# Kernel optimization log

Measured on AMD Instinct MI355X. Metric: run time of the kernel, lower is better.

Reference implementation:

```python
import jax, jax.numpy as jnp
import numpy as np

SEQ_LEN = 4096
DIM = 256  # hidden_dim, must be even


def rope_tables(seq_len, dim):
    half = dim // 2
    pos = jnp.arange(seq_len, dtype=jnp.float32)[:, None]  # (s,1)
    div = jnp.exp(jnp.arange(half, dtype=jnp.float32) * (-jnp.log(jnp.float32(10000.0)) / half))
    ang = pos * div  # (s, half)
    return jnp.sin(ang), jnp.cos(ang)


def apply_rope(x, sin, cos):
    # x: (b, s, d); sin/cos: (s, d//2). Interleaved pair rotation.
    b, s, d = x.shape
    xp = x.reshape(b, s, d // 2, 2)
    x_even, x_odd = xp[..., 0], xp[..., 1]
    out_even = x_even * cos - x_odd * sin
    out_odd = x_even * sin + x_odd * cos
    return jnp.stack([out_even, out_odd], axis=-1).reshape(b, s, d)


def setup_inputs() -> dict:
    key = jax.random.key(0)
    k1, k2, k3, k4 = jax.random.split(key, 4)
    x = jax.random.normal(k1, (4, SEQ_LEN, DIM), dtype=jnp.float32)
    W0 = jax.random.normal(k2, (DIM, DIM), dtype=jnp.float32)
    W1 = jax.random.normal(k3, (DIM, DIM), dtype=jnp.float32)
    W2 = jax.random.normal(k4, (DIM, DIM), dtype=jnp.float32)
    return {"x": x, "W0": W0, "W1": W1, "W2": W2}


def reference(x, W0, W1, W2):
    sin, cos = rope_tables(x.shape[1], W0.shape[1])
    x0 = apply_rope(jnp.einsum('bsi,ih->bsh', x, W0), sin, cos)  # (b,s,h)
    x1 = apply_rope(jnp.einsum('bsi,ih->bsh', x, W1), sin, cos)  # (b,s,h)
    scores = jnp.einsum('bsh,bth->bst', x0, x1)                   # (b,s,s)
    attn = jax.nn.softmax(scores, axis=-1)
    x2 = jnp.einsum('bsh,ho->bso', x, W2)                         # (b,s,o)
    out = jnp.einsum('bst,bto->bso', attn, x2)
    return out[:, 0, :]
```

## Files before the change

kernel.cpp:

```cpp
#include <hip/hip_runtime.h>
#include <math.h>

#define BB 4
#define SS 4096
#define DD 256
#define WT_PLANE 65536

typedef __attribute__((ext_vector_type(8))) _Float16 h8v;
typedef __attribute__((ext_vector_type(4))) float f4v;

__device__ __forceinline__ ushort f2h(float f) {
    _Float16 h = (_Float16)f;
    return __builtin_bit_cast(ushort, h);
}
__device__ __forceinline__ float h2f(ushort u) {
    return (float)__builtin_bit_cast(_Float16, u);
}
__device__ __forceinline__ void split2htwo(float a, float b, uint& h, uint& l) {
    const ushort ah = f2h(a);
    const ushort al = f2h(a - h2f(ah));
    const ushort bh = f2h(b);
    const ushort bl = f2h(b - h2f(bh));
    h = (uint)ah | ((uint)bh << 16);
    l = (uint)al | ((uint)bl << 16);
}

__global__ __launch_bounds__(256) void prep_kernel(const float* __restrict__ x,
                                                   const float* __restrict__ W0,
                                                   const float* __restrict__ W1,
                                                   float* __restrict__ q,
                                                   float* __restrict__ y,
                                                   float* __restrict__ out,
                                                   ushort* __restrict__ wt,
                                                   float* __restrict__ cs) {
    __shared__ float sh[64 * 65];
    const int bid = blockIdx.x;
    const int tid = threadIdx.x;

    if (bid < 2048) {
        const int t = ((bid & 63) << 6) | (tid & 63);
        const int j = ((bid >> 6) << 2) | (tid >> 6);
        const float kfac = (float)(-9.210340371976184 / 128.0);
        const float d = expf((float)j * kfac);
        float sv, cv;
        sincosf((float)t * d, &sv, &cv);
        *(float2*)(cs + ((size_t)j * SS + t) * 2) = make_float2(cv, sv);
    } else if (bid < 2080) {
        const int qb = bid - 2048;
        const int b = qb >> 3;
        const int hc = qb & 7;
        if (hc == 0) y[b * DD + tid] = 0.f;
        if (hc == 1) out[b * DD + tid] = 0.f;
        const int hk = tid & 31;
        const int iseg = tid >> 5;
        const int h = hc * 32 + hk;
        const float* xrow = x + (size_t)b * SS * DD;
        float p = 0.f;
#pragma unroll
        for (int k = 0; k < 32; ++k) {
            const int i = iseg * 32 + k;
            p = fmaf(xrow[i], W0[i * DD + h], p);
        }
        sh[tid] = p;
        __syncthreads();
        if (tid < 32) {
            float s = 0.f;
#pragma unroll
            for (int jj = 0; jj < 8; ++jj) s += sh[jj * 32 + tid];
            q[b * DD + hc * 32 + tid] = s;
        }
    } else {
        const int cb = bid - 2080;
        const int k0 = (cb & 3) * 64;
        const int c0 = (cb >> 2) * 64;
        {
            const int kr = tid >> 2;
            const int csg = tid & 3;
            const float* src = W1 + (size_t)(k0 + kr) * DD + c0 + csg * 16;
#pragma unroll
            for (int i = 0; i < 4; ++i) {
                const float4 v = *(const float4*)(src + i * 4);
                sh[kr * 65 + csg * 16 + i * 4 + 0] = v.x;
                sh[kr * 65 + csg * 16 + i * 4 + 1] = v.y;
                sh[kr * 65 + csg * 16 + i * 4 + 2] = v.z;
                sh[kr * 65 + csg * 16 + i * 4 + 3] = v.w;
            }
        }
        __syncthreads();
        {
            const int cr = tid >> 2;
            const int ks2 = tid & 3;
            const int c = c0 + cr;
#pragma unroll
            for (int oct = 0; oct < 2; ++oct) {
                const int k = k0 + ks2 * 16 + oct * 8;
                const int kl = ks2 * 16 + oct * 8;
                uint H[4], L[4];
#pragma unroll
                for (int i = 0; i < 4; ++i) {
                    const float fa = sh[(kl + 2 * i + 0) * 65 + cr];
                    const float fb = sh[(kl + 2 * i + 1) * 65 + cr];
                    split2htwo(fa, fb, H[i], L[i]);
                }
                const size_t idx = ((size_t)(c >> 4) * 8 + (k >> 5)) * 512
                                 + (size_t)((k >> 3) & 3) * 128 + (size_t)(c & 15) * 8;
                *(uint4*)(wt + idx) = make_uint4(H[0], H[1], H[2], H[3]);
                *(uint4*)(wt + WT_PLANE + idx) = make_uint4(L[0], L[1], L[2], L[3]);
            }
        }
    }
}

__global__ __launch_bounds__(1024, 4) void scores_mfma(const float* __restrict__ x,
                                                       const ushort* __restrict__ wt,
                                                       const float* __restrict__ q,
                                                       const float* __restrict__ cs,
                                                       float* __restrict__ scores) {
    __shared__ __align__(16) unsigned char smem[65536];
    __shared__ float scomb[8][64];
    __shared__ float q_s[256];
    const int tid = threadIdx.x;
    const int bid = blockIdx.x;
    const int b = bid >> 6;
    const int row0 = (bid & 63) << 6;

    if (tid < 256) q_s[tid] = q[b * DD + tid];

    {
        const int r = tid >> 4;
        const int seg = tid & 15;
        const float* xr = x + ((size_t)(b * SS + row0 + r)) * DD + seg * 16;
        const int swz = (r & 15) << 4;
#pragma unroll
        for (int j = 0; j < 2; ++j) {
            const float4 f0 = *(const float4*)(xr + j * 8);
            const float4 f1 = *(const float4*)(xr + j * 8 + 4);
            uint H[4], L[4];
            split2htwo(f0.x, f0.y, H[0], L[0]);
            split2htwo(f0.z, f0.w, H[1], L[1]);
            split2htwo(f1.x, f1.y, H[2], L[2]);
            split2htwo(f1.z, f1.w, H[3], L[3]);
            const int s = seg * 2 + j;
            const int off = r * 512 + (((s << 4)) ^ swz);
            *(uint4*)(smem + off) = make_uint4(H[0], H[1], H[2], H[3]);
            *(uint4*)(smem + 32768 + off) = make_uint4(L[0], L[1], L[2], L[3]);
        }
    }
    __syncthreads();

    const int lane = tid & 63;
    const int wv = tid >> 6;
    const int rh = wv >> 3;
    const int cg = wv & 7;
    const int l15 = lane & 15;
    const int hg = lane >> 4;

    f4v acc[2][2];
#pragma unroll
    for (int rt = 0; rt < 2; ++rt)
#pragma unroll
        for (int ct = 0; ct < 2; ++ct) acc[rt][ct] = {0.f, 0.f, 0.f, 0.f};

    const ushort* wb = wt + (size_t)lane * 8;
    const int aswz = l15 << 4;

#pragma unroll
    for (int ks = 0; ks < 8; ++ks) {
        h8v a_h[2], a_l[2];
#pragma unroll
        for (int rt = 0; rt < 2; ++rt) {
            const int row = rh * 32 + rt * 16 + l15;
            const int off = row * 512 + ((((ks * 4 + hg) << 4)) ^ aswz);
            a_h[rt] = *(const h8v*)(smem + off);
            a_l[rt] = *(const h8v*)(smem + 32768 + off);
        }
#pragma unroll
        for (int ct = 0; ct < 2; ++ct) {
            const int gct = cg * 2 + ct;
            const ushort* bp = wb + (size_t)(gct * 8 + ks) * 512;
            const h8v b_h = *(const h8v*)(bp);
            const h8v b_l = *(const h8v*)(bp + WT_PLANE);
#pragma unroll
            for (int rt = 0; rt < 2; ++rt) {
                acc[rt][ct] = __builtin_amdgcn_mfma_f32_16x16x32_f16(a_h[rt], b_h, acc[rt][ct], 0, 0, 0);
                acc[rt][ct] = __builtin_amdgcn_mfma_f32_16x16x32_f16(a_h[rt], b_l, acc[rt][ct], 0, 0, 0);
                acc[rt][ct] = __builtin_amdgcn_mfma_f32_16x16x32_f16(a_l[rt], b_h, acc[rt][ct], 0, 0, 0);
            }
        }
    }

    const int par = l15 & 1;
    float p[2][4];
#pragma unroll
    for (int rt = 0; rt < 2; ++rt)
#pragma unroll
        for (int i = 0; i < 4; ++i) p[rt][i] = 0.f;

#pragma unroll
    for (int ct = 0; ct < 2; ++ct) {
        const int c = (cg * 2 + ct) * 16 + l15;
        const int j = c >> 1;
        const float qe = q_s[2 * j], qo = q_s[2 * j + 1];
        const float* csp = cs + (size_t)j * (SS * 2);
#pragma unroll
        for (int rt = 0; rt < 2; ++rt) {
            const int t0 = row0 + rh * 32 + rt * 16 + hg * 4;
            const float4 csA = *(const float4*)(csp + t0 * 2);
            const float4 csB = *(const float4*)(csp + t0 * 2 + 4);
            const float u0 = par ? (qo * csA.x - qe * csA.y) : (qe * csA.x + qo * csA.y);
            const float u1 = par ? (qo * csA.z - qe * csA.w) : (qe * csA.z + qo * csA.w);
            const float u2 = par ? (qo * csB.x - qe * csB.y) : (qe * csB.x + qo * csB.y);
            const float u3 = par ? (qo * csB.z - qe * csB.w) : (qe * csB.z + qo * csB.w);
            p[rt][0] = fmaf(acc[rt][ct][0], u0, p[rt][0]);
            p[rt][1] = fmaf(acc[rt][ct][1], u1, p[rt][1]);
            p[rt][2] = fmaf(acc[rt][ct][2], u2, p[rt][2]);
            p[rt][3] = fmaf(acc[rt][ct][3], u3, p[rt][3]);
        }
    }
#pragma unroll
    for (int rt = 0; rt < 2; ++rt) {
#pragma unroll
        for (int off = 1; off <= 8; off <<= 1) {
            p[rt][0] += __shfl_xor(p[rt][0], off);
            p[rt][1] += __shfl_xor(p[rt][1], off);
            p[rt][2] += __shfl_xor(p[rt][2], off);
            p[rt][3] += __shfl_xor(p[rt][3], off);
        }
        if (l15 == 0)
            *(float4*)&scomb[cg][rh * 32 + rt * 16 + hg * 4] =
                make_float4(p[rt][0], p[rt][1], p[rt][2], p[rt][3]);
    }
    __syncthreads();
    if (tid < 64) {
        float s = 0.f;
#pragma unroll
        for (int g = 0; g < 8; ++g) s += scomb[g][tid];
        scores[(size_t)b * SS + row0 + tid] = s;
    }
}

__global__ __launch_bounds__(256) void fused_kernel(const float* __restrict__ x,
                                                    const float* __restrict__ scores,
                                                    float* __restrict__ y) {
    const int c = blockIdx.x;
    const int b = blockIdx.y;
    const int tid = threadIdx.x;
    const int lane = tid & 63;
    const int wid = tid >> 6;
    const float* sb = scores + (size_t)b * SS;

    float4 v[4];
    float m = -INFINITY;
#pragma unroll
    for (int i = 0; i < 4; ++i) {
        v[i] = *(const float4*)(sb + tid * 16 + i * 4);
        m = fmaxf(m, fmaxf(fmaxf(v[i].x, v[i].y), fmaxf(v[i].z, v[i].w)));
    }
#pragma unroll
    for (int off = 32; off >= 1; off >>= 1) m = fmaxf(m, __shfl_xor(m, off));
    __shared__ float redm[4];
    __shared__ float reds[4];
    __shared__ float a_s[64];
    if (lane == 0) redm[wid] = m;
    __syncthreads();
    const float M = fmaxf(fmaxf(redm[0], redm[1]), fmaxf(redm[2], redm[3]));

    float s = 0.f;
#pragma unroll
    for (int i = 0; i < 4; ++i) {
        s += expf(v[i].x - M);
        s += expf(v[i].y - M);
        s += expf(v[i].z - M);
        s += expf(v[i].w - M);
    }
#pragma unroll
    for (int off = 32; off >= 1; off >>= 1) s += __shfl_xor(s, off);
    if (lane == 0) reds[wid] = s;
    __syncthreads();
    const float S = ((reds[0] + reds[1]) + reds[2]) + reds[3];
    const float inv = 1.0f / S;

    if (tid < 64) a_s[tid] = expf(sb[c * 64 + tid] - M) * inv;
    __syncthreads();

    float accv = 0.f;
    for (int t = 0; t < 64; ++t) {
        const float a = a_s[t];
        if (a != 0.f)
            accv = fmaf(a, x[((size_t)(b * SS + c * 64 + t)) * DD + tid], accv);
    }
    atomicAdd(&y[b * DD + tid], accv);
}

__global__ __launch_bounds__(256) void out_kernel(const float* __restrict__ y,
                                                  const float* __restrict__ W2,
                                                  float* __restrict__ out) {
    const int i0 = blockIdx.x * 16;
    const int b = blockIdx.y;
    const int o = threadIdx.x;
    __shared__ float y_s[16];
    if (o < 16) y_s[o] = y[b * DD + i0 + o];
    __syncthreads();
    float p = 0.f;
#pragma unroll
    for (int ii = 0; ii < 16; ++ii) p = fmaf(y_s[ii], W2[(size_t)(i0 + ii) * DD + o], p);
    atomicAdd(&out[b * DD + o], p);
}

extern "C" void kernel_launch(void* const* d_in, const int* in_sizes, int n_in,
                              void* d_out, int out_size, void* d_ws, size_t ws_size,
                              hipStream_t stream) {
    const float* x = (const float*)d_in[0];
    const float* W0 = (const float*)d_in[1];
    const float* W1 = (const float*)d_in[2];
    const float* W2 = (const float*)d_in[3];
    float* ws = (float*)d_ws;
    float* q = ws;
    float* scores = ws + 1024;
    float* y = ws + 17408;
    ushort* wt = (ushort*)(ws + 18432);
    float* cs = ws + 116736;
    float* out = (float*)d_out;

    prep_kernel<<<dim3(2096), 256, 0, stream>>>(x, W0, W1, q, y, out, wt, cs);
    scores_mfma<<<dim3(256), 1024, 0, stream>>>(x, wt, q, cs, scores);
    fused_kernel<<<dim3(64, BB), 256, 0, stream>>>(x, scores, y);
    out_kernel<<<dim3(16, BB), 256, 0, stream>>>(y, W2, out);
}
```

Baseline: 31.01 us.

## Compute RoPE sin/cos tables in LDS inside scores kernel, split weight conversion

The global sin/cos table (128x4096 pairs) is no longer built in the prep kernel and stored to global memory. Each scores block now computes the 128x64 slice it needs directly into LDS, and all x loads are issued before that transcendental work to hide their latency. The W1 fp16 split conversion moves into its own small kernel, which adds a launch but shrinks the prep grid from 2096 to 32 blocks. Every scores block (256 in total) recomputes its sincos values, and the extra ~66KB of LDS may reduce occupancy of the 1024-thread blocks.

```diff
diff --git a/kernel.cpp b/kernel.cpp
--- a/kernel.cpp
+++ b/kernel.cpp
@@ -30,25 +30,14 @@
                                                    const float* __restrict__ W1,
                                                    float* __restrict__ q,
                                                    float* __restrict__ y,
-                                                   float* __restrict__ out,
-                                                   ushort* __restrict__ wt,
-                                                   float* __restrict__ cs) {
+                                                   float* __restrict__ out) {
     __shared__ float sh[64 * 65];
     const int bid = blockIdx.x;
     const int tid = threadIdx.x;
 
-    if (bid < 2048) {
-        const int t = ((bid & 63) << 6) | (tid & 63);
-        const int j = ((bid >> 6) << 2) | (tid >> 6);
-        const float kfac = (float)(-9.210340371976184 / 128.0);
-        const float d = expf((float)j * kfac);
-        float sv, cv;
-        sincosf((float)t * d, &sv, &cv);
-        *(float2*)(cs + ((size_t)j * SS + t) * 2) = make_float2(cv, sv);
-    } else if (bid < 2080) {
-        const int qb = bid - 2048;
-        const int b = qb >> 3;
-        const int hc = qb & 7;
+    if (bid < 32) {
+        const int b = bid >> 3;
+        const int hc = bid & 7;
         if (hc == 0) y[b * DD + tid] = 0.f;
         if (hc == 1) out[b * DD + tid] = 0.f;
         const int hk = tid & 31;
@@ -70,43 +59,49 @@
             q[b * DD + hc * 32 + tid] = s;
         }
     } else {
-        const int cb = bid - 2080;
-        const int k0 = (cb & 3) * 64;
-        const int c0 = (cb >> 2) * 64;
-        {
-            const int kr = tid >> 2;
-            const int csg = tid & 3;
-            const float* src = W1 + (size_t)(k0 + kr) * DD + c0 + csg * 16;
+    }
+}
+
+__global__ __launch_bounds__(256) void convert_kernel(const float* __restrict__ W1,
+                                                      ushort* __restrict__ wt) {
+    __shared__ float sh[64 * 65];
+    const int cb = blockIdx.x;
+    const int tid = threadIdx.x;
+    const int k0 = (cb & 3) * 64;
+    const int c0 = (cb >> 2) * 64;
+    {
+        const int kr = tid >> 2;
+        const int csg = tid & 3;
+        const float* src = W1 + (size_t)(k0 + kr) * DD + c0 + csg * 16;
+#pragma unroll
+        for (int i = 0; i < 4; ++i) {
+            const float4 v = *(const float4*)(src + i * 4);
+            sh[kr * 65 + csg * 16 + i * 4 + 0] = v.x;
+            sh[kr * 65 + csg * 16 + i * 4 + 1] = v.y;
+            sh[kr * 65 + csg * 16 + i * 4 + 2] = v.z;
+            sh[kr * 65 + csg * 16 + i * 4 + 3] = v.w;
+        }
+    }
+    __syncthreads();
+    {
+        const int cr = tid >> 2;
+        const int ks2 = tid & 3;
+        const int c = c0 + cr;
+#pragma unroll
+        for (int oct = 0; oct < 2; ++oct) {
+            const int k = k0 + ks2 * 16 + oct * 8;
+            const int kl = ks2 * 16 + oct * 8;
+            uint H[4], L[4];
 #pragma unroll
             for (int i = 0; i < 4; ++i) {
-                const float4 v = *(const float4*)(src + i * 4);
-                sh[kr * 65 + csg * 16 + i * 4 + 0] = v.x;
-                sh[kr * 65 + csg * 16 + i * 4 + 1] = v.y;
-                sh[kr * 65 + csg * 16 + i * 4 + 2] = v.z;
-                sh[kr * 65 + csg * 16 + i * 4 + 3] = v.w;
+                const float fa = sh[(kl + 2 * i + 0) * 65 + cr];
+                const float fb = sh[(kl + 2 * i + 1) * 65 + cr];
+                split2htwo(fa, fb, H[i], L[i]);
             }
-        }
-        __syncthreads();
-        {
-            const int cr = tid >> 2;
-            const int ks2 = tid & 3;
-            const int c = c0 + cr;
-#pragma unroll
-            for (int oct = 0; oct < 2; ++oct) {
-                const int k = k0 + ks2 * 16 + oct * 8;
-                const int kl = ks2 * 16 + oct * 8;
-                uint H[4], L[4];
-#pragma unroll
-                for (int i = 0; i < 4; ++i) {
-                    const float fa = sh[(kl + 2 * i + 0) * 65 + cr];
-                    const float fb = sh[(kl + 2 * i + 1) * 65 + cr];
-                    split2htwo(fa, fb, H[i], L[i]);
-                }
-                const size_t idx = ((size_t)(c >> 4) * 8 + (k >> 5)) * 512
-                                 + (size_t)((k >> 3) & 3) * 128 + (size_t)(c & 15) * 8;
-                *(uint4*)(wt + idx) = make_uint4(H[0], H[1], H[2], H[3]);
-                *(uint4*)(wt + WT_PLANE + idx) = make_uint4(L[0], L[1], L[2], L[3]);
-            }
+            const size_t idx = ((size_t)(c >> 4) * 8 + (k >> 5)) * 512
+                             + (size_t)((k >> 3) & 3) * 128 + (size_t)(c & 15) * 8;
+            *(uint4*)(wt + idx) = make_uint4(H[0], H[1], H[2], H[3]);
+            *(uint4*)(wt + WT_PLANE + idx) = make_uint4(L[0], L[1], L[2], L[3]);
         }
     }
 }
@@ -114,9 +109,9 @@
 __global__ __launch_bounds__(1024, 4) void scores_mfma(const float* __restrict__ x,
                                                        const ushort* __restrict__ wt,
                                                        const float* __restrict__ q,
-                                                       const float* __restrict__ cs,
                                                        float* __restrict__ scores) {
     __shared__ __align__(16) unsigned char smem[65536];
+    __shared__ __align__(16) float cs_lds[128 * 132];
     __shared__ float scomb[8][64];
     __shared__ float q_s[256];
     const int tid = threadIdx.x;
@@ -124,27 +119,49 @@
     const int b = bid >> 6;
     const int row0 = (bid & 63) << 6;
 
+    const int r = tid >> 4;
+    const int seg = tid & 15;
+    const float* xr = x + ((size_t)(b * SS + row0 + r)) * DD + seg * 16;
+    float4 xf0 = *(const float4*)(xr);
+    float4 xf1 = *(const float4*)(xr + 4);
+    float4 xf2 = *(const float4*)(xr + 8);
+    float4 xf3 = *(const float4*)(xr + 12);
+
+    {
+        const float kfac = (float)(-9.210340371976184 / 128.0);
+        const int jj = tid >> 3;
+        const int tl0 = (tid & 7) * 8;
+        const float d = expf((float)jj * kfac);
+        float* dst = cs_lds + jj * 132 + tl0 * 2;
+#pragma unroll
+        for (int e = 0; e < 8; ++e) {
+            float sv, cv;
+            sincosf((float)(row0 + tl0 + e) * d, &sv, &cv);
+            dst[2 * e] = cv;
+            dst[2 * e + 1] = sv;
+        }
+    }
     if (tid < 256) q_s[tid] = q[b * DD + tid];
 
     {
-        const int r = tid >> 4;
-        const int seg = tid & 15;
-        const float* xr = x + ((size_t)(b * SS + row0 + r)) * DD + seg * 16;
         const int swz = (r & 15) << 4;
-#pragma unroll
-        for (int j = 0; j < 2; ++j) {
-            const float4 f0 = *(const float4*)(xr + j * 8);
-            const float4 f1 = *(const float4*)(xr + j * 8 + 4);
-            uint H[4], L[4];
-            split2htwo(f0.x, f0.y, H[0], L[0]);
-            split2htwo(f0.z, f0.w, H[1], L[1]);
-            split2htwo(f1.x, f1.y, H[2], L[2]);
-            split2htwo(f1.z, f1.w, H[3], L[3]);
-            const int s = seg * 2 + j;
-            const int off = r * 512 + (((s << 4)) ^ swz);
-            *(uint4*)(smem + off) = make_uint4(H[0], H[1], H[2], H[3]);
-            *(uint4*)(smem + 32768 + off) = make_uint4(L[0], L[1], L[2], L[3]);
-        }
+        uint H[4], L[4];
+        split2htwo(xf0.x, xf0.y, H[0], L[0]);
+        split2htwo(xf0.z, xf0.w, H[1], L[1]);
+        split2htwo(xf1.x, xf1.y, H[2], L[2]);
+        split2htwo(xf1.z, xf1.w, H[3], L[3]);
+        int s = seg * 2;
+        int off = r * 512 + (((s << 4)) ^ swz);
+        *(uint4*)(smem + off) = make_uint4(H[0], H[1], H[2], H[3]);
+        *(uint4*)(smem + 32768 + off) = make_uint4(L[0], L[1], L[2], L[3]);
+        split2htwo(xf2.x, xf2.y, H[0], L[0]);
+        split2htwo(xf2.z, xf2.w, H[1], L[1]);
+        split2htwo(xf3.x, xf3.y, H[2], L[2]);
+        split2htwo(xf3.z, xf3.w, H[3], L[3]);
+        s = seg * 2 + 1;
+        off = r * 512 + (((s << 4)) ^ swz);
+        *(uint4*)(smem + off) = make_uint4(H[0], H[1], H[2], H[3]);
+        *(uint4*)(smem + 32768 + off) = make_uint4(L[0], L[1], L[2], L[3]);
     }
     __syncthreads();
 
@@ -201,12 +218,12 @@
         const int c = (cg * 2 + ct) * 16 + l15;
         const int j = c >> 1;
         const float qe = q_s[2 * j], qo = q_s[2 * j + 1];
-        const float* csp = cs + (size_t)j * (SS * 2);
+        const float* csp = cs_lds + j * 132;
 #pragma unroll
         for (int rt = 0; rt < 2; ++rt) {
-            const int t0 = row0 + rh * 32 + rt * 16 + hg * 4;
-            const float4 csA = *(const float4*)(csp + t0 * 2);
-            const float4 csB = *(const float4*)(csp + t0 * 2 + 4);
+            const int tloc = rh * 32 + rt * 16 + hg * 4;
+            const float4 csA = *(const float4*)(csp + tloc * 2);
+            const float4 csB = *(const float4*)(csp + tloc * 2 + 4);
             const float u0 = par ? (qo * csA.x - qe * csA.y) : (qe * csA.x + qo * csA.y);
             const float u1 = par ? (qo * csA.z - qe * csA.w) : (qe * csA.z + qo * csA.w);
             const float u2 = par ? (qo * csB.x - qe * csB.y) : (qe * csB.x + qo * csB.y);
@@ -319,11 +336,11 @@
     float* scores = ws + 1024;
     float* y = ws + 17408;
     ushort* wt = (ushort*)(ws + 18432);
-    float* cs = ws + 116736;
     float* out = (float*)d_out;
 
-    prep_kernel<<<dim3(2096), 256, 0, stream>>>(x, W0, W1, q, y, out, wt, cs);
-    scores_mfma<<<dim3(256), 1024, 0, stream>>>(x, wt, q, cs, scores);
+    prep_kernel<<<dim3(32), 256, 0, stream>>>(x, W0, W1, q, y, out);
+    convert_kernel<<<dim3(16), 256, 0, stream>>>(W1, wt);
+    scores_mfma<<<dim3(256), 1024, 0, stream>>>(x, wt, q, scores);
     fused_kernel<<<dim3(64, BB), 256, 0, stream>>>(x, scores, y);
     out_kernel<<<dim3(16, BB), 256, 0, stream>>>(y, W2, out);
 }
```

Result: slower. 32.59 us (+5.1%).

## Fuse softmax stats into scores kernel and merge attention-weighted sum with W2 projection

Applied to the files above, without the earlier changes.

The scores kernel now emits a per-64-row partial (max, sum-exp) pair, so the softmax reduction no longer rescans all 4096 scores in every block. The attention-weighted sum and the W2 output projection are merged into one 1024-thread kernel. Each block applies W2 to its own partial y chunk and atomically adds the result into out, which removes one launch and the intermediate y buffer. The cost is that every one of the 256 blocks now reads the full W2 matrix instead of a slice of it. Blocks whose attention weights are all zero exit early, which skips most of the x and W2 traffic when the softmax is peaked.

```diff
diff --git a/kernel.cpp b/kernel.cpp
--- a/kernel.cpp
+++ b/kernel.cpp
@@ -29,7 +29,6 @@
                                                    const float* __restrict__ W0,
                                                    const float* __restrict__ W1,
                                                    float* __restrict__ q,
-                                                   float* __restrict__ y,
                                                    float* __restrict__ out,
                                                    ushort* __restrict__ wt,
                                                    float* __restrict__ cs) {
@@ -49,8 +48,7 @@
         const int qb = bid - 2048;
         const int b = qb >> 3;
         const int hc = qb & 7;
-        if (hc == 0) y[b * DD + tid] = 0.f;
-        if (hc == 1) out[b * DD + tid] = 0.f;
+        if (hc == 0) out[b * DD + tid] = 0.f;
         const int hk = tid & 31;
         const int iseg = tid >> 5;
         const int h = hc * 32 + hk;
@@ -115,7 +113,8 @@
                                                        const ushort* __restrict__ wt,
                                                        const float* __restrict__ q,
                                                        const float* __restrict__ cs,
-                                                       float* __restrict__ scores) {
+                                                       float* __restrict__ scores,
+                                                       float2* __restrict__ partials) {
     __shared__ __align__(16) unsigned char smem[65536];
     __shared__ float scomb[8][64];
     __shared__ float q_s[256];
@@ -236,75 +235,75 @@
 #pragma unroll
         for (int g = 0; g < 8; ++g) s += scomb[g][tid];
         scores[(size_t)b * SS + row0 + tid] = s;
-    }
-}
-
-__global__ __launch_bounds__(256) void fused_kernel(const float* __restrict__ x,
-                                                    const float* __restrict__ scores,
-                                                    float* __restrict__ y) {
+        float m = s;
+#pragma unroll
+        for (int off = 32; off >= 1; off >>= 1) m = fmaxf(m, __shfl_xor(m, off));
+        float sc = expf(s - m);
+#pragma unroll
+        for (int off = 32; off >= 1; off >>= 1) sc += __shfl_xor(sc, off);
+        if (tid == 0) partials[(b << 6) + (bid & 63)] = make_float2(m, sc);
+    }
+}
+
+__global__ __launch_bounds__(1024) void final_kernel(const float* __restrict__ x,
+                                                     const float* __restrict__ scores,
+                                                     const float2* __restrict__ partials,
+                                                     const float* __restrict__ W2,
+                                                     float* __restrict__ out) {
     const int c = blockIdx.x;
     const int b = blockIdx.y;
     const int tid = threadIdx.x;
-    const int lane = tid & 63;
-    const int wid = tid >> 6;
-    const float* sb = scores + (size_t)b * SS;
-
-    float4 v[4];
-    float m = -INFINITY;
-#pragma unroll
-    for (int i = 0; i < 4; ++i) {
-        v[i] = *(const float4*)(sb + tid * 16 + i * 4);
-        m = fmaxf(m, fmaxf(fmaxf(v[i].x, v[i].y), fmaxf(v[i].z, v[i].w)));
-    }
-#pragma unroll
-    for (int off = 32; off >= 1; off >>= 1) m = fmaxf(m, __shfl_xor(m, off));
-    __shared__ float redm[4];
-    __shared__ float reds[4];
     __shared__ float a_s[64];
-    if (lane == 0) redm[wid] = m;
-    __syncthreads();
-    const float M = fmaxf(fmaxf(redm[0], redm[1]), fmaxf(redm[2], redm[3]));
-
-    float s = 0.f;
-#pragma unroll
-    for (int i = 0; i < 4; ++i) {
-        s += expf(v[i].x - M);
-        s += expf(v[i].y - M);
-        s += expf(v[i].z - M);
-        s += expf(v[i].w - M);
-    }
-#pragma unroll
-    for (int off = 32; off >= 1; off >>= 1) s += __shfl_xor(s, off);
-    if (lane == 0) reds[wid] = s;
-    __syncthreads();
-    const float S = ((reds[0] + reds[1]) + reds[2]) + reds[3];
-    const float inv = 1.0f / S;
-
-    if (tid < 64) a_s[tid] = expf(sb[c * 64 + tid] - M) * inv;
-    __syncthreads();
-
+    __shared__ float yls[4][256];
+    __shared__ float MS[2];
+    __shared__ int flag;
+    if (tid == 0) flag = 0;
+
+    if (tid < 64) {
+        const float2 pp = partials[(b << 6) + tid];
+        float m = pp.x;
+#pragma unroll
+        for (int off = 32; off >= 1; off >>= 1) m = fmaxf(m, __shfl_xor(m, off));
+        float sc = pp.y * expf(pp.x - m);
+#pragma unroll
+        for (int off = 32; off >= 1; off >>= 1) sc += __shfl_xor(sc, off);
+        if (tid == 0) {
+            MS[0] = m;
+            MS[1] = sc;
+        }
+    }
+    __syncthreads();
+    const float M = MS[0];
+    const float inv = 1.0f / MS[1];
+
+    if (tid < 64) {
+        const float a = expf(scores[(size_t)b * SS + (c << 6) + tid] - M) * inv;
+        a_s[tid] = a;
+        if (__any(a != 0.f) && tid == 0) flag = 1;
+    }
+    __syncthreads();
+    if (!flag) return;
+
+    const int o = tid & 255;
+    const int th = tid >> 8;
     float accv = 0.f;
-    for (int t = 0; t < 64; ++t) {
+#pragma unroll
+    for (int t = th * 16; t < th * 16 + 16; ++t) {
         const float a = a_s[t];
         if (a != 0.f)
-            accv = fmaf(a, x[((size_t)(b * SS + c * 64 + t)) * DD + tid], accv);
-    }
-    atomicAdd(&y[b * DD + tid], accv);
-}
-
-__global__ __launch_bounds__(256) void out_kernel(const float* __restrict__ y,
-                                                  const float* __restrict__ W2,
-                                                  float* __restrict__ out) {
-    const int i0 = blockIdx.x * 16;
-    const int b = blockIdx.y;
-    const int o = threadIdx.x;
-    __shared__ float y_s[16];
-    if (o < 16) y_s[o] = y[b * DD + i0 + o];
-    __syncthreads();
-    float p = 0.f;
-#pragma unroll
-    for (int ii = 0; ii < 16; ++ii) p = fmaf(y_s[ii], W2[(size_t)(i0 + ii) * DD + o], p);
-    atomicAdd(&out[b * DD + o], p);
+            accv = fmaf(a, x[((size_t)(b * SS + c * 64 + t)) * DD + o], accv);
+    }
+    yls[th][o] = accv;
+    __syncthreads();
+
+    float pr = 0.f;
+#pragma unroll 8
+    for (int ii = 0; ii < 64; ++ii) {
+        const int i = th * 64 + ii;
+        const float yv = ((yls[0][i] + yls[1][i]) + yls[2][i]) + yls[3][i];
+        pr = fmaf(yv, W2[(size_t)i * DD + o], pr);
+    }
+    atomicAdd(&out[b * DD + o], pr);
 }
 
 extern "C" void kernel_launch(void* const* d_in, const int* in_sizes, int n_in,
@@ -317,13 +316,12 @@
     float* ws = (float*)d_ws;
     float* q = ws;
     float* scores = ws + 1024;
-    float* y = ws + 17408;
+    float2* partials = (float2*)(ws + 17408);
     ushort* wt = (ushort*)(ws + 18432);
     float* cs = ws + 116736;
     float* out = (float*)d_out;
 
-    prep_kernel<<<dim3(2096), 256, 0, stream>>>(x, W0, W1, q, y, out, wt, cs);
-    scores_mfma<<<dim3(256), 1024, 0, stream>>>(x, wt, q, cs, scores);
-    fused_kernel<<<dim3(64, BB), 256, 0, stream>>>(x, scores, y);
-    out_kernel<<<dim3(16, BB), 256, 0, stream>>>(y, W2, out);
-}
+    prep_kernel<<<dim3(2096), 256, 0, stream>>>(x, W0, W1, q, out, wt, cs);
+    scores_mfma<<<dim3(256), 1024, 0, stream>>>(x, wt, q, cs, scores, partials);
+    final_kernel<<<dim3(64, BB), 1024, 0, stream>>>(x, scores, partials, W2, out);
+}
```

New measurement: 28.35 us. 8.6% less time.
